# Kernel optimization log

Measured on AMD Instinct MI355X. Metric: run time of the kernel, lower is better.

## Reference

```python
import jax, jax.numpy as jnp
import numpy as np

LAM = 0.5          # lambda_ in DyGCN
GROUPS = 4
EPS_GN = 1e-5
EPS_LN = 1e-5


def _group_norm(y, w, b):
    # y: [B, Ch, N, T]; GroupNorm over (channels-in-group, N, T)
    B, Ch, N, T = y.shape
    yr = y.reshape(B, GROUPS, Ch // GROUPS, N, T)
    mu = yr.mean(axis=(2, 3, 4), keepdims=True)
    var = yr.var(axis=(2, 3, 4), keepdims=True)
    yn = ((yr - mu) * jax.lax.rsqrt(var + EPS_GN)).reshape(B, Ch, N, T)
    return yn * w[None, :, None, None] + b[None, :, None, None]


def _gtu(X, w, b, pw, pb, qw, qb):
    # grouped conv2d, kernel (1,k), stride 1, VALID; out channels = 2*H
    xc = jax.lax.conv_general_dilated(
        X, w, window_strides=(1, 1), padding='VALID',
        feature_group_count=GROUPS,
        dimension_numbers=('NCHW', 'OIHW', 'NCHW'))
    xc = xc + b[None, :, None, None]
    H = X.shape[1]
    xp = _group_norm(xc[:, :H], pw, pb)   # matches torch chunk(2, dim=1)
    xq = _group_norm(xc[:, H:], qw, qb)
    mish = xp * jnp.tanh(jax.nn.softplus(xp))   # Mish
    gate = jnp.clip(xq, 0.0, 1.0)               # Hardtanh(0,1)
    return mish * gate


def reference(x, static_adj, U1, U2, U3, be, Ve, W0, b0, masks, Ws, bs, Wd, bd,
              conv3_w, conv5_w, conv7_w, conv9_w, conv_b,
              gn_pw, gn_pb, gn_qw, gn_qb, fc_w, fc_b, res_w, res_b, ln_w, ln_b):
    B, N, C, T = x.shape
    # ---- Temporal attention ----
    lhs = jnp.einsum('btc,cn->btn', jnp.einsum('bnct,n->btc', x, U1), U2)  # [B,T,N]
    rhs = jnp.einsum('c,bnct->bnt', U3, x)                                 # [B,N,T]
    product = jnp.einsum('btn,bns->bts', lhs, rhs)                          # [B,T,T]
    E = jnp.einsum('ij,bjk->bik', Ve, jax.nn.sigmoid(product + be))
    At = jax.nn.softmax(E, axis=1)
    x_TAt = jnp.einsum('bmt,bts->bms', x.reshape(B, N * C, T), At).reshape(B, N, C, T)
    # ---- DyGCN, vectorized across T ----
    xt = jnp.moveaxis(x_TAt, -1, 1)                                        # [B,T,N,C]
    x0 = jnp.einsum('btnc,hc->btnh', xt, W0) + b0                          # shared linear
    enh = static_adj[None] * jax.nn.sigmoid(masks)                         # [T,N,N]
    s = jnp.einsum('tnm,btmc->btnc', enh, xt)
    static_out = jnp.einsum('btnc,thc->btnh', s, Ws) + bs[None, :, None, :]
    # dynamic branch (DynamicGCNLayer): data-dependent adjacency
    scores = jnp.einsum('btnc,btmc->btnm', xt, xt) / jnp.sqrt(jnp.float32(C))
    adj = jax.nn.softmax(scores, axis=-1)                                  # [B,T,N,N]
    d = jnp.einsum('btnm,btmc->btnc', adj, xt)
    dyn_out = jnp.einsum('btnc,thc->btnh', d, Wd) + bd[None, :, None, :]
    fused = (LAM - 0.025) * static_out + (1.0 - LAM - 0.025) * dyn_out + 0.05 * x0
    X = jnp.transpose(fused, (0, 3, 2, 1))                                 # [B,H,N,T]
    # ---- multi-scale gated temporal convs ----
    outs = [
        _gtu(X, conv3_w, conv_b[0], gn_pw[0], gn_pb[0], gn_qw[0], gn_qb[0]),
        _gtu(X, conv5_w, conv_b[1], gn_pw[1], gn_pb[1], gn_qw[1], gn_qb[1]),
        _gtu(X, conv7_w, conv_b[2], gn_pw[2], gn_pb[2], gn_qw[2], gn_qb[2]),
        _gtu(X, conv9_w, conv_b[3], gn_pw[3], gn_pb[3], gn_qw[3], gn_qb[3]),
    ]
    tc = jnp.concatenate(outs, axis=-1)                                    # [B,H,N,4T-20]
    tc = jnp.einsum('bhnk,ok->bhno', tc, fc_w) + fc_b                      # fcmy (dropout=eval no-op)
    tco = jax.nn.relu(tc)                                                  # [B,H,N,T]
    # ---- residual + LayerNorm ----
    residual = jnp.einsum('bnct,hc->bhnt', x, res_w) + res_b[None, :, None, None]
    y = jax.nn.relu(residual + tco)                                        # [B,H,N,T]
    yp = jnp.transpose(y, (0, 3, 2, 1))                                    # [B,T,N,H]
    mu = yp.mean(axis=-1, keepdims=True)
    var = yp.var(axis=-1, keepdims=True)
    yn = (yp - mu) * jax.lax.rsqrt(var + EPS_LN) * ln_w + ln_b
    return jnp.transpose(yn, (0, 2, 3, 1))                                 # [B,N,H,T]


def setup_inputs():
    key = jax.random.key(0)
    ks = jax.random.split(key, 32)
    B, N, C, T, H = 16, 512, 64, 12, 64
    w = 0.05
    A = jax.random.uniform(ks[0], (N, N), jnp.float32)
    A = A / A.sum(axis=-1, keepdims=True)  # row-normalized static adjacency
    return {
        'x': jax.random.normal(ks[1], (B, N, C, T), jnp.float32),
        'static_adj': A,
        'U1': jax.random.normal(ks[2], (N,), jnp.float32) * w,
        'U2': jax.random.normal(ks[3], (C, N), jnp.float32) * w,
        'U3': jax.random.normal(ks[4], (C,), jnp.float32) * w,
        'be': jax.random.normal(ks[5], (1, T, T), jnp.float32) * w,
        'Ve': jax.random.normal(ks[6], (T, T), jnp.float32) * w,
        'W0': jax.random.normal(ks[7], (H, C), jnp.float32) * w,
        'b0': jnp.zeros((H,), jnp.float32),
        'masks': jax.random.uniform(ks[8], (T, N, N), jnp.float32, 0.8, 1.2),
        'Ws': jax.random.normal(ks[9], (T, H, C), jnp.float32) * w,
        'bs': jnp.zeros((T, H), jnp.float32),
        'Wd': jax.random.normal(ks[10], (T, H, C), jnp.float32) * w,
        'bd': jnp.zeros((T, H), jnp.float32),
        'conv3_w': jax.random.normal(ks[11], (2 * H, H // 4, 1, 3), jnp.float32) * w,
        'conv5_w': jax.random.normal(ks[12], (2 * H, H // 4, 1, 5), jnp.float32) * w,
        'conv7_w': jax.random.normal(ks[13], (2 * H, H // 4, 1, 7), jnp.float32) * w,
        'conv9_w': jax.random.normal(ks[14], (2 * H, H // 4, 1, 9), jnp.float32) * w,
        'conv_b': jnp.zeros((4, 2 * H), jnp.float32),
        'gn_pw': jnp.ones((4, H), jnp.float32),
        'gn_pb': jnp.zeros((4, H), jnp.float32),
        'gn_qw': jnp.ones((4, H), jnp.float32),
        'gn_qb': jnp.zeros((4, H), jnp.float32),
        'fc_w': jax.random.normal(ks[15], (T, 4 * T - 20), jnp.float32) * w,
        'fc_b': jnp.zeros((T,), jnp.float32),
        'res_w': jax.random.normal(ks[16], (H, C), jnp.float32) * w,
        'res_b': jnp.zeros((H,), jnp.float32),
        'ln_w': jnp.ones((H,), jnp.float32),
        'ln_b': jnp.zeros((H,), jnp.float32),
    }
```

## Files before the change

kernel.cpp:

```cpp
#include <hip/hip_runtime.h>

constexpr int Bb = 16, Nn = 512, Cc = 64, Tt = 12, Hh = 64;
constexpr int NCT = Nn * Cc * Tt;
constexpr int CT  = Cc * Tt;

__global__ void k0_rest(const float* __restrict__ rw, float* __restrict__ resT) {
    int i = blockIdx.x * 256 + threadIdx.x;
    if (i < Hh * Cc) {
        int h = i >> 6, c = i & 63;
        resT[c * 64 + h] = rw[i];
    }
}

__global__ void k1a_tmp1(const float* __restrict__ x, const float* __restrict__ U1,
                         float* __restrict__ tmp1) {
    int blk = blockIdx.x;
    int b = blk / 12; int r = blk % 12;
    int ctb = r >> 2; int nch = r & 3;
    int ct = ctb * 256 + threadIdx.x;
    const float* xb = x + (size_t)b * NCT;
    float acc = 0.f;
    int n0 = nch * 128;
    for (int n = n0; n < n0 + 128; ++n)
        acc += xb[n * CT + ct] * U1[n];
    atomicAdd(&tmp1[b * CT + ct], acc);
}

__global__ void k1b_rhs(const float* __restrict__ x, const float* __restrict__ U3,
                        float* __restrict__ rhs) {
    int wid = blockIdx.x * 4 + (threadIdx.x >> 6);
    int b = wid >> 9; int n = wid & 511;
    int l = threadIdx.x & 63;
    const float4* x4 = (const float4*)(x + (size_t)(b * Nn + n) * CT);
    float4 a0 = x4[3 * l], a1 = x4[3 * l + 1], a2 = x4[3 * l + 2];
    float xv[12] = {a0.x,a0.y,a0.z,a0.w, a1.x,a1.y,a1.z,a1.w, a2.x,a2.y,a2.z,a2.w};
    float u = U3[l];
    float p[12];
    #pragma unroll
    for (int t = 0; t < 12; ++t) p[t] = u * xv[t];
    #pragma unroll
    for (int off = 1; off < 64; off <<= 1) {
        #pragma unroll
        for (int t = 0; t < 12; ++t) p[t] += __shfl_xor(p[t], off);
    }
    if (l == 0) {
        float* rp = rhs + (size_t)(b * Nn + n) * 12;
        *(float4*)(rp)     = make_float4(p[0], p[1], p[2], p[3]);
        *(float4*)(rp + 4) = make_float4(p[4], p[5], p[6], p[7]);
        *(float4*)(rp + 8) = make_float4(p[8], p[9], p[10], p[11]);
    }
}

__global__ void k1c_lhs(const float* __restrict__ tmp1, const float* __restrict__ U2,
                        float* __restrict__ lhG) {
    __shared__ float t1[CT];
    int b = blockIdx.x >> 1; int nn = (blockIdx.x & 1) * 256 + threadIdx.x;
    for (int i = threadIdx.x; i < CT; i += 256) t1[i] = tmp1[b * CT + i];
    __syncthreads();
    float l[Tt];
    #pragma unroll
    for (int t = 0; t < Tt; ++t) l[t] = 0.f;
    for (int c = 0; c < Cc; ++c) {
        float u2 = U2[c * Nn + nn];
        #pragma unroll
        for (int t = 0; t < Tt; ++t) l[t] += t1[c * Tt + t] * u2;
    }
    #pragma unroll
    for (int t = 0; t < Tt; ++t) lhG[(size_t)(b * Tt + t) * Nn + nn] = l[t];
}

__global__ void k1c_att(const float* __restrict__ lhG, const float* __restrict__ rhs,
                        const float* __restrict__ be, const float* __restrict__ Ve,
                        float* __restrict__ At) {
    __shared__ float rh[Nn * Tt];
    __shared__ float lh[Tt * Nn];
    __shared__ float part[576];
    __shared__ float sp[144];
    __shared__ float Ee[144];
    int b = blockIdx.x, tid = threadIdx.x;
    for (int i = tid; i < Nn * Tt; i += 256) rh[i] = rhs[b * Nn * Tt + i];
    for (int i = tid; i < Tt * Nn; i += 256) lh[i] = lhG[(size_t)b * Tt * Nn + i];
    __syncthreads();
    for (int task = tid; task < 576; task += 256) {
        int ts = task >> 2, ch = task & 3;
        int t = ts / 12, s2 = ts % 12;
        int n0 = ch * 128;
        float a = 0.f;
        for (int nn = n0; nn < n0 + 128; ++nn) a += lh[t * Nn + nn] * rh[nn * Tt + s2];
        part[task] = a;
    }
    __syncthreads();
    if (tid < 144) {
        float a = part[tid * 4] + part[tid * 4 + 1] + part[tid * 4 + 2] + part[tid * 4 + 3]
                + be[tid];
        sp[tid] = 1.f / (1.f + __expf(-a));
    }
    __syncthreads();
    if (tid < 144) {
        int i = tid / 12, k = tid % 12;
        float a = 0.f;
        #pragma unroll
        for (int j = 0; j < 12; ++j) a += Ve[i * 12 + j] * sp[j * 12 + k];
        Ee[tid] = a;
    }
    __syncthreads();
    if (tid < 12) {
        int k = tid;
        float mx = -1e30f;
        #pragma unroll
        for (int i = 0; i < 12; ++i) mx = fmaxf(mx, Ee[i * 12 + k]);
        float su = 0.f; float ex[12];
        #pragma unroll
        for (int i = 0; i < 12; ++i) { ex[i] = __expf(Ee[i * 12 + k] - mx); su += ex[i]; }
        float inv = 1.f / su;
        #pragma unroll
        for (int i = 0; i < 12; ++i) At[b * 144 + i * 12 + k] = ex[i] * inv;
    }
}

__global__ void k2_xtt(const float* __restrict__ x, const float* __restrict__ At,
                       float* __restrict__ xtN) {
    int idx = blockIdx.x * 256 + threadIdx.x;
    int c = idx & 63; int n = (idx >> 6) & 511; int b = idx >> 15;
    const float4* x4 = (const float4*)(x + (size_t)((b * Nn + n) * Cc + c) * Tt);
    float4 a0 = x4[0], a1 = x4[1], a2 = x4[2];
    float xv[12] = {a0.x,a0.y,a0.z,a0.w, a1.x,a1.y,a1.z,a1.w, a2.x,a2.y,a2.z,a2.w};
    const float* Ab = At + b * 144;
    float* op = xtN + (size_t)b * Tt * Nn * Cc + n * Cc + c;
    #pragma unroll
    for (int t = 0; t < Tt; ++t) {
        float a = 0.f;
        #pragma unroll
        for (int u = 0; u < Tt; ++u) a += xv[u] * Ab[u * 12 + t];
        op[(size_t)t * Nn * Cc] = a;
    }
}

__global__ void k2b_enh(const float* __restrict__ adj, const float* __restrict__ masks,
                        float* __restrict__ enhT) {
    __shared__ float tile[32][33];
    int blk = blockIdx.x;
    int t = blk >> 8; int r = blk & 255;
    int n0 = (r >> 4) * 32; int m0 = (r & 15) * 32;
    int tx = threadIdx.x & 31; int ty = threadIdx.x >> 5;
    #pragma unroll
    for (int i = 0; i < 4; ++i) {
        int nl = ty + 8 * i;
        float a  = adj[(n0 + nl) * Nn + m0 + tx];
        float mk = masks[t * Nn * Nn + (n0 + nl) * Nn + m0 + tx];
        tile[nl][tx] = a / (1.f + __expf(-mk));
    }
    __syncthreads();
    #pragma unroll
    for (int i = 0; i < 4; ++i) {
        int ml = ty + 8 * i;
        enhT[(size_t)(t * Nn + m0 + ml) * Nn + n0 + tx] = tile[tx][ml];
    }
}

__global__ __launch_bounds__(256) __attribute__((amdgpu_waves_per_eu(1, 3)))
void k3_gcn(
    const float* __restrict__ xtN, const float* __restrict__ enhT,
    const float* __restrict__ W0, const float* __restrict__ b0,
    const float* __restrict__ Ws, const float* __restrict__ bs,
    const float* __restrict__ Wd, const float* __restrict__ bd,
    float* __restrict__ F) {
    __shared__ float xs[64][64];
    int blk = (blockIdx.x & 7) * 96 + (blockIdx.x >> 3);
    int seg = blk & 3; int t = (blk >> 2) % Tt; int b = blk / 48;
    int tid = threadIdx.x;
    int lane = tid & 63;
    int w = tid >> 6;
    int half = lane >> 5;
    int r = lane & 31;
    int n = seg * 128 + w * 32 + r;
    int c0 = half * 32;
    const float* xb = xtN + (size_t)(b * Tt + t) * Nn * Cc;
    float row[32];
    {
        const float4* r4 = (const float4*)(xb + n * Cc + c0);
        #pragma unroll
        for (int jj = 0; jj < 8; ++jj) {
            float4 a = r4[jj];
            row[jj*4] = a.x; row[jj*4+1] = a.y; row[jj*4+2] = a.z; row[jj*4+3] = a.w;
        }
    }
    float accd[32], accs[32];
    #pragma unroll
    for (int j = 0; j < 32; ++j) { accd[j] = 0.f; accs[j] = 0.f; }
    float sumexp = 0.f;
    const float* eh = enhT + (size_t)t * Nn * Nn + n;
    for (int m0 = 0; m0 < Nn; m0 += 64) {
        __syncthreads();
        {
            const float4* src = (const float4*)(xb + m0 * Cc);
            float4* dst = (float4*)&xs[0][0];
            #pragma unroll
            for (int i = 0; i < 4; ++i) dst[i * 256 + tid] = src[i * 256 + tid];
        }
        __syncthreads();
        #pragma unroll 1
        for (int m = 0; m < 64; ++m) {
            const float4* vp = (const float4*)&xs[m][c0];
            float4 v0 = vp[0], v1 = vp[1], v2 = vp[2], v3 = vp[3];
            float4 v4 = vp[4], v5 = vp[5], v6 = vp[6], v7 = vp[7];
            float sa, sb;
            sa = row[0]*v0.x + row[1]*v0.y + row[2]*v0.z + row[3]*v0.w
               + row[4]*v1.x + row[5]*v1.y + row[6]*v1.z + row[7]*v1.w
               + row[8]*v2.x + row[9]*v2.y + row[10]*v2.z + row[11]*v2.w
               + row[12]*v3.x + row[13]*v3.y + row[14]*v3.z + row[15]*v3.w;
            sb = row[16]*v4.x + row[17]*v4.y + row[18]*v4.z + row[19]*v4.w
               + row[20]*v5.x + row[21]*v5.y + row[22]*v5.z + row[23]*v5.w
               + row[24]*v6.x + row[25]*v6.y + row[26]*v6.z + row[27]*v6.w
               + row[28]*v7.x + row[29]*v7.y + row[30]*v7.z + row[31]*v7.w;
            float s = sa + sb;
            s += __shfl_xor(s, 32);
            float p = __expf(s * 0.125f);
            sumexp += p;
            float e = eh[(size_t)(m0 + m) * Nn];
            accd[0]  += p*v0.x; accd[1]  += p*v0.y; accd[2]  += p*v0.z; accd[3]  += p*v0.w;
            accd[4]  += p*v1.x; accd[5]  += p*v1.y; accd[6]  += p*v1.z; accd[7]  += p*v1.w;
            accd[8]  += p*v2.x; accd[9]  += p*v2.y; accd[10] += p*v2.z; accd[11] += p*v2.w;
            accd[12] += p*v3.x; accd[13] += p*v3.y; accd[14] += p*v3.z; accd[15] += p*v3.w;
            accd[16] += p*v4.x; accd[17] += p*v4.y; accd[18] += p*v4.z; accd[19] += p*v4.w;
            accd[20] += p*v5.x; accd[21] += p*v5.y; accd[22] += p*v5.z; accd[23] += p*v5.w;
            accd[24] += p*v6.x; accd[25] += p*v6.y; accd[26] += p*v6.z; accd[27] += p*v6.w;
            accd[28] += p*v7.x; accd[29] += p*v7.y; accd[30] += p*v7.z; accd[31] += p*v7.w;
            accs[0]  += e*v0.x; accs[1]  += e*v0.y; accs[2]  += e*v0.z; accs[3]  += e*v0.w;
            accs[4]  += e*v1.x; accs[5]  += e*v1.y; accs[6]  += e*v1.z; accs[7]  += e*v1.w;
            accs[8]  += e*v2.x; accs[9]  += e*v2.y; accs[10] += e*v2.z; accs[11] += e*v2.w;
            accs[12] += e*v3.x; accs[13] += e*v3.y; accs[14] += e*v3.z; accs[15] += e*v3.w;
            accs[16] += e*v4.x; accs[17] += e*v4.y; accs[18] += e*v4.z; accs[19] += e*v4.w;
            accs[20] += e*v5.x; accs[21] += e*v5.y; accs[22] += e*v5.z; accs[23] += e*v5.w;
            accs[24] += e*v6.x; accs[25] += e*v6.y; accs[26] += e*v6.z; accs[27] += e*v6.w;
            accs[28] += e*v7.x; accs[29] += e*v7.y; accs[30] += e*v7.z; accs[31] += e*v7.w;
        }
    }
    float invd = 0.475f / sumexp;
    #pragma unroll
    for (int j = 0; j < 32; ++j) {
        accd[j] *= invd; accs[j] *= 0.475f; row[j] *= 0.05f;
    }
    const float* Wst = Ws + t * Hh * Cc;
    const float* Wdt = Wd + t * Hh * Cc;
    float* Fp = F + ((size_t)(b * Tt + t) * Nn + n) * Hh;
    for (int hb = 0; hb < 16; ++hb) {
        float oo[4];
        #pragma unroll
        for (int k = 0; k < 4; ++k) {
            int h = hb * 4 + k;
            const float4* w04 = (const float4*)(W0 + h * Cc + c0);
            const float4* ws4 = (const float4*)(Wst + h * Cc + c0);
            const float4* wd4 = (const float4*)(Wdt + h * Cc + c0);
            float a = 0.f;
            #pragma unroll
            for (int jj = 0; jj < 8; ++jj) {
                float4 wv = w04[jj], sv = ws4[jj], dv = wd4[jj];
                a += row[jj*4+0]*wv.x + row[jj*4+1]*wv.y + row[jj*4+2]*wv.z + row[jj*4+3]*wv.w;
                a += accs[jj*4+0]*sv.x + accs[jj*4+1]*sv.y + accs[jj*4+2]*sv.z + accs[jj*4+3]*sv.w;
                a += accd[jj*4+0]*dv.x + accd[jj*4+1]*dv.y + accd[jj*4+2]*dv.z + accd[jj*4+3]*dv.w;
            }
            a += __shfl_xor(a, 32);
            oo[k] = a + 0.05f * b0[h] + 0.475f * (bs[t * Hh + h] + bd[t * Hh + h]);
        }
        if ((hb >> 3) == half)
            *(float4*)(Fp + hb * 4) = make_float4(oo[0], oo[1], oo[2], oo[3]);
    }
}

__global__ __launch_bounds__(512) void k4_conv(
                        const float* __restrict__ F,
                        const float* __restrict__ w3, const float* __restrict__ w5,
                        const float* __restrict__ w7, const float* __restrict__ w9,
                        const float* __restrict__ cb,
                        float* __restrict__ xc, float* __restrict__ stats) {
    __shared__ float fl[4 * Tt * Hh];
    __shared__ float sstat[64];
    int blk = blockIdx.x;
    int b = blk >> 7; int n0 = (blk & 127) * 4;
    int tid = threadIdx.x;
    if (tid < 64) sstat[tid] = 0.f;
    for (int i = tid; i < 3072; i += 512) {
        int t = i >> 8; int r = i & 255;
        fl[i] = F[(size_t)(b * Tt + t) * Nn * Hh + n0 * Hh + r];
    }
    __syncthreads();
    int nl = tid >> 7; int co = tid & 127;
    int g = co >> 5;
    float a3[10], a5[8], a7[6], a9[4];
    {
        float c3 = cb[co], c5 = cb[128 + co], c7 = cb[256 + co], c9 = cb[384 + co];
        #pragma unroll
        for (int j = 0; j < 10; ++j) a3[j] = c3;
        #pragma unroll
        for (int j = 0; j < 8; ++j) a5[j] = c5;
        #pragma unroll
        for (int j = 0; j < 6; ++j) a7[j] = c7;
        #pragma unroll
        for (int j = 0; j < 4; ++j) a9[j] = c9;
    }
    for (int ci = 0; ci < 16; ++ci) {
        int cig = g * 16 + ci;
        float xr[12];
        #pragma unroll
        for (int tt = 0; tt < 12; ++tt) xr[tt] = fl[tt * 256 + nl * 64 + cig];
        const float* p3 = w3 + (co * 16 + ci) * 3;
        #pragma unroll
        for (int dt = 0; dt < 3; ++dt) {
            float wv = p3[dt];
            #pragma unroll
            for (int j = 0; j < 10; ++j) a3[j] += xr[j + dt] * wv;
        }
        const float* p5 = w5 + (co * 16 + ci) * 5;
        #pragma unroll
        for (int dt = 0; dt < 5; ++dt) {
            float wv = p5[dt];
            #pragma unroll
            for (int j = 0; j < 8; ++j) a5[j] += xr[j + dt] * wv;
        }
        const float* p7 = w7 + (co * 16 + ci) * 7;
        #pragma unroll
        for (int dt = 0; dt < 7; ++dt) {
            float wv = p7[dt];
            #pragma unroll
            for (int j = 0; j < 6; ++j) a7[j] += xr[j + dt] * wv;
        }
        const float* p9 = w9 + (co * 16 + ci) * 9;
        #pragma unroll
        for (int dt = 0; dt < 9; ++dt) {
            float wv = p9[dt];
            #pragma unroll
            for (int j = 0; j < 4; ++j) a9[j] += xr[j + dt] * wv;
        }
    }
    int pg = (co < 64) ? (co >> 4) : 4 + ((co - 64) >> 4);
    float* xcw = xc + (size_t)(b * Nn + n0 + nl) * 28 * 128 + co;
    float su, sq;
    su = 0.f; sq = 0.f;
    #pragma unroll
    for (int j = 0; j < 10; ++j) { float v = a3[j]; xcw[j * 128] = v; su += v; sq += v * v; }
    #pragma unroll
    for (int off = 1; off < 16; off <<= 1) { su += __shfl_xor(su, off); sq += __shfl_xor(sq, off); }
    if ((tid & 15) == 0) { atomicAdd(&sstat[(0 * 8 + pg) * 2], su); atomicAdd(&sstat[(0 * 8 + pg) * 2 + 1], sq); }
    su = 0.f; sq = 0.f;
    #pragma unroll
    for (int j = 0; j < 8; ++j) { float v = a5[j]; xcw[(10 + j) * 128] = v; su += v; sq += v * v; }
    #pragma unroll
    for (int off = 1; off < 16; off <<= 1) { su += __shfl_xor(su, off); sq += __shfl_xor(sq, off); }
    if ((tid & 15) == 0) { atomicAdd(&sstat[(1 * 8 + pg) * 2], su); atomicAdd(&sstat[(1 * 8 + pg) * 2 + 1], sq); }
    su = 0.f; sq = 0.f;
    #pragma unroll
    for (int j = 0; j < 6; ++j) { float v = a7[j]; xcw[(18 + j) * 128] = v; su += v; sq += v * v; }
    #pragma unroll
    for (int off = 1; off < 16; off <<= 1) { su += __shfl_xor(su, off); sq += __shfl_xor(sq, off); }
    if ((tid & 15) == 0) { atomicAdd(&sstat[(2 * 8 + pg) * 2], su); atomicAdd(&sstat[(2 * 8 + pg) * 2 + 1], sq); }
    su = 0.f; sq = 0.f;
    #pragma unroll
    for (int j = 0; j < 4; ++j) { float v = a9[j]; xcw[(24 + j) * 128] = v; su += v; sq += v * v; }
    #pragma unroll
    for (int off = 1; off < 16; off <<= 1) { su += __shfl_xor(su, off); sq += __shfl_xor(sq, off); }
    if ((tid & 15) == 0) { atomicAdd(&sstat[(3 * 8 + pg) * 2], su); atomicAdd(&sstat[(3 * 8 + pg) * 2 + 1], sq); }
    __syncthreads();
    if (tid < 64) {
        int s = tid >> 4; int pgq = (tid >> 1) & 7; int st = tid & 1;
        atomicAdd(&stats[((s * Bb + b) * 8 + pgq) * 2 + st], sstat[(s * 8 + pgq) * 2 + st]);
    }
}

__global__ __launch_bounds__(256) void k5_final(
                         const float* __restrict__ xc, const float* __restrict__ stats,
                         const float* __restrict__ x,
                         const float* __restrict__ gpw, const float* __restrict__ gpb,
                         const float* __restrict__ gqw, const float* __restrict__ gqb,
                         const float* __restrict__ fcw, const float* __restrict__ fcb,
                         const float* __restrict__ resT, const float* __restrict__ rb,
                         const float* __restrict__ lnw, const float* __restrict__ lnb,
                         float* __restrict__ out) {
    int blk = blockIdx.x;
    int b = blk >> 7; int n = (blk & 127) * 4 + (threadIdx.x >> 6);
    int h = threadIdx.x & 63;
    int pg = h >> 4;
    const int TkA[4] = {10, 8, 6, 4};
    float mu_p[4], rs_p[4], mu_q[4], rs_q[4];
    #pragma unroll
    for (int s = 0; s < 4; ++s) {
        float cnt = 16.f * 512.f * (float)TkA[s];
        float su = stats[((s * Bb + b) * 8 + pg) * 2];
        float sq = stats[((s * Bb + b) * 8 + pg) * 2 + 1];
        float mu = su / cnt; float var = sq / cnt - mu * mu;
        mu_p[s] = mu; rs_p[s] = rsqrtf(var + 1e-5f);
        su = stats[((s * Bb + b) * 8 + 4 + pg) * 2];
        sq = stats[((s * Bb + b) * 8 + 4 + pg) * 2 + 1];
        mu = su / cnt; var = sq / cnt - mu * mu;
        mu_q[s] = mu; rs_q[s] = rsqrtf(var + 1e-5f);
    }
    const float* xcp = xc + (size_t)(b * Nn + n) * 28 * 128;
    float pb_[28], qb_[28];
    #pragma unroll
    for (int k = 0; k < 28; ++k) {
        pb_[k] = xcp[k * 128 + h];
        qb_[k] = xcp[k * 128 + 64 + h];
    }
    float tc[28];
    int off = 0;
    #pragma unroll
    for (int s = 0; s < 4; ++s) {
        float pw = gpw[s * 64 + h], pbv = gpb[s * 64 + h];
        float qw = gqw[s * 64 + h], qbv = gqb[s * 64 + h];
        #pragma unroll
        for (int j = 0; j < 10; ++j) {
            if (j < TkA[s]) {
                float p = (pb_[off + j] - mu_p[s]) * rs_p[s] * pw + pbv;
                float q = (qb_[off + j] - mu_q[s]) * rs_q[s] * qw + qbv;
                float mish;
                if (p > 20.f) mish = p;
                else { float z = 1.f + __expf(p); float z2 = z * z; mish = p * (z2 - 1.f) / (z2 + 1.f); }
                float gate = fminf(fmaxf(q, 0.f), 1.f);
                tc[off + j] = mish * gate;
            }
        }
        off += TkA[s];
    }
    float o[12];
    #pragma unroll
    for (int t = 0; t < 12; ++t) {
        float a = fcb[t];
        #pragma unroll
        for (int k = 0; k < 28; ++k) a += tc[k] * fcw[t * 28 + k];
        o[t] = fmaxf(a, 0.f);
    }
    const float* xr = x + (size_t)(b * Nn + n) * CT;
    float res[12];
    float rbv = rb[h];
    #pragma unroll
    for (int t = 0; t < 12; ++t) res[t] = rbv;
    for (int c = 0; c < 64; ++c) {
        float rv = resT[c * 64 + h];
        #pragma unroll
        for (int t = 0; t < 12; ++t) res[t] += xr[c * 12 + t] * rv;
    }
    float y[12];
    #pragma unroll
    for (int t = 0; t < 12; ++t) y[t] = fmaxf(res[t] + o[t], 0.f);
    float lw = lnw[h], lb = lnb[h];
    float ov[12];
    #pragma unroll
    for (int t = 0; t < 12; ++t) {
        float s1 = y[t], s2 = y[t] * y[t];
        #pragma unroll
        for (int o2 = 32; o2 > 0; o2 >>= 1) {
            s1 += __shfl_xor(s1, o2);
            s2 += __shfl_xor(s2, o2);
        }
        float mu = s1 * (1.f / 64.f);
        float var = s2 * (1.f / 64.f) - mu * mu;
        ov[t] = (y[t] - mu) * rsqrtf(var + 1e-5f) * lw + lb;
    }
    float* op = out + ((size_t)(b * Nn + n) * Hh + h) * Tt;
    *(float4*)(op)     = make_float4(ov[0], ov[1], ov[2], ov[3]);
    *(float4*)(op + 4) = make_float4(ov[4], ov[5], ov[6], ov[7]);
    *(float4*)(op + 8) = make_float4(ov[8], ov[9], ov[10], ov[11]);
}

extern "C" void kernel_launch(void* const* d_in, const int* in_sizes, int n_in,
                              void* d_out, int out_size, void* d_ws, size_t ws_size,
                              hipStream_t stream) {
    const float* x    = (const float*)d_in[0];
    const float* adj  = (const float*)d_in[1];
    const float* U1   = (const float*)d_in[2];
    const float* U2   = (const float*)d_in[3];
    const float* U3   = (const float*)d_in[4];
    const float* be   = (const float*)d_in[5];
    const float* Ve   = (const float*)d_in[6];
    const float* W0   = (const float*)d_in[7];
    const float* b0   = (const float*)d_in[8];
    const float* masks= (const float*)d_in[9];
    const float* Ws   = (const float*)d_in[10];
    const float* bs   = (const float*)d_in[11];
    const float* Wd   = (const float*)d_in[12];
    const float* bd   = (const float*)d_in[13];
    const float* w3   = (const float*)d_in[14];
    const float* w5   = (const float*)d_in[15];
    const float* w7   = (const float*)d_in[16];
    const float* w9   = (const float*)d_in[17];
    const float* cb   = (const float*)d_in[18];
    const float* gpw  = (const float*)d_in[19];
    const float* gpb  = (const float*)d_in[20];
    const float* gqw  = (const float*)d_in[21];
    const float* gqb  = (const float*)d_in[22];
    const float* fcw  = (const float*)d_in[23];
    const float* fcb  = (const float*)d_in[24];
    const float* rw   = (const float*)d_in[25];
    const float* rb   = (const float*)d_in[26];
    const float* lnw  = (const float*)d_in[27];
    const float* lnb  = (const float*)d_in[28];
    float* out = (float*)d_out;
    float* ws  = (float*)d_ws;

    float* tmp1  = ws;
    float* stats = ws + 12288;
    float* At    = ws + 13312;
    float* rhs   = ws + 15616;
    float* resT  = ws + 113920;
    float* xtN   = ws + 118016;
    float* enhT  = ws + 6409472;
    float* F     = ws + 9555200;
    float* xc    = ws + 15846656;
    float* lhG   = xtN;

    hipMemsetAsync(ws, 0, 13312 * sizeof(float), stream);

    k0_rest<<<16, 256, 0, stream>>>(rw, resT);
    k1a_tmp1<<<192, 256, 0, stream>>>(x, U1, tmp1);
    k1b_rhs<<<2048, 256, 0, stream>>>(x, U3, rhs);
    k2b_enh<<<3072, 256, 0, stream>>>(adj, masks, enhT);
    k1c_lhs<<<32, 256, 0, stream>>>(tmp1, U2, lhG);
    k1c_att<<<16, 256, 0, stream>>>(lhG, rhs, be, Ve, At);
    k2_xtt<<<2048, 256, 0, stream>>>(x, At, xtN);
    k3_gcn<<<768, 256, 0, stream>>>(xtN, enhT, W0, b0, Ws, bs, Wd, bd, F);
    k4_conv<<<2048, 512, 0, stream>>>(F, w3, w5, w7, w9, cb, xc, stats);
    k5_final<<<2048, 256, 0, stream>>>(xc, stats, x, gpw, gpb, gqw, gqb,
                                       fcw, fcb, resT, rb, lnw, lnb, out);
}
```

Before: 1.405 ms.

## Split GCN channels four ways per node and stage enhanced adjacency in LDS

The GCN kernel now gives each node to four lanes with 16 channels each instead of two lanes with 32, halving per-thread accumulator registers. The grid doubles to 1536 blocks of 64 nodes, and the occupancy hint is raised to 4 waves per EU. The enhanced-adjacency tile is now loaded cooperatively into shared memory with float4 loads instead of strided per-thread global reads. In exchange there is an extra shuffle per reduction, twice the xs tile reloads across blocks, and more LDS per block.

```diff
diff --git a/kernel.cpp b/kernel.cpp
--- a/kernel.cpp
+++ b/kernel.cpp
@@ -158,7 +158,7 @@
     }
 }
 
-__global__ __launch_bounds__(256) __attribute__((amdgpu_waves_per_eu(1, 3)))
+__global__ __launch_bounds__(256) __attribute__((amdgpu_waves_per_eu(4)))
 void k3_gcn(
     const float* __restrict__ xtN, const float* __restrict__ enhT,
     const float* __restrict__ W0, const float* __restrict__ b0,
@@ -166,30 +166,32 @@
     const float* __restrict__ Wd, const float* __restrict__ bd,
     float* __restrict__ F) {
     __shared__ float xs[64][64];
-    int blk = (blockIdx.x & 7) * 96 + (blockIdx.x >> 3);
-    int seg = blk & 3; int t = (blk >> 2) % Tt; int b = blk / 48;
+    __shared__ float es[64][64];
+    int blk = (blockIdx.x & 7) * 192 + (blockIdx.x >> 3);
+    int seg = blk & 7; int t = (blk >> 3) % Tt; int b = blk / 96;
     int tid = threadIdx.x;
     int lane = tid & 63;
     int w = tid >> 6;
-    int half = lane >> 5;
-    int r = lane & 31;
-    int n = seg * 128 + w * 32 + r;
-    int c0 = half * 32;
+    int cg = lane >> 4;
+    int r = lane & 15;
+    int nl = w * 16 + r;
+    int n = seg * 64 + nl;
+    int c0 = cg * 16;
     const float* xb = xtN + (size_t)(b * Tt + t) * Nn * Cc;
-    float row[32];
+    const float* eb = enhT + (size_t)t * Nn * Nn + seg * 64;
+    float row[16];
     {
         const float4* r4 = (const float4*)(xb + n * Cc + c0);
         #pragma unroll
-        for (int jj = 0; jj < 8; ++jj) {
+        for (int jj = 0; jj < 4; ++jj) {
             float4 a = r4[jj];
             row[jj*4] = a.x; row[jj*4+1] = a.y; row[jj*4+2] = a.z; row[jj*4+3] = a.w;
         }
     }
-    float accd[32], accs[32];
-    #pragma unroll
-    for (int j = 0; j < 32; ++j) { accd[j] = 0.f; accs[j] = 0.f; }
+    float accd[16], accs[16];
+    #pragma unroll
+    for (int j = 0; j < 16; ++j) { accd[j] = 0.f; accs[j] = 0.f; }
     float sumexp = 0.f;
-    const float* eh = enhT + (size_t)t * Nn * Nn + n;
     for (int m0 = 0; m0 < Nn; m0 += 64) {
         __syncthreads();
         {
@@ -198,47 +200,44 @@
             #pragma unroll
             for (int i = 0; i < 4; ++i) dst[i * 256 + tid] = src[i * 256 + tid];
         }
+        {
+            #pragma unroll
+            for (int i = 0; i < 4; ++i) {
+                int f = i * 256 + tid;
+                int m = f >> 4; int q = f & 15;
+                *(float4*)&es[m][q * 4] =
+                    *(const float4*)(eb + (size_t)(m0 + m) * Nn + q * 4);
+            }
+        }
         __syncthreads();
         #pragma unroll 1
         for (int m = 0; m < 64; ++m) {
             const float4* vp = (const float4*)&xs[m][c0];
             float4 v0 = vp[0], v1 = vp[1], v2 = vp[2], v3 = vp[3];
-            float4 v4 = vp[4], v5 = vp[5], v6 = vp[6], v7 = vp[7];
             float sa, sb;
             sa = row[0]*v0.x + row[1]*v0.y + row[2]*v0.z + row[3]*v0.w
-               + row[4]*v1.x + row[5]*v1.y + row[6]*v1.z + row[7]*v1.w
-               + row[8]*v2.x + row[9]*v2.y + row[10]*v2.z + row[11]*v2.w
+               + row[4]*v1.x + row[5]*v1.y + row[6]*v1.z + row[7]*v1.w;
+            sb = row[8]*v2.x + row[9]*v2.y + row[10]*v2.z + row[11]*v2.w
                + row[12]*v3.x + row[13]*v3.y + row[14]*v3.z + row[15]*v3.w;
-            sb = row[16]*v4.x + row[17]*v4.y + row[18]*v4.z + row[19]*v4.w
-               + row[20]*v5.x + row[21]*v5.y + row[22]*v5.z + row[23]*v5.w
-               + row[24]*v6.x + row[25]*v6.y + row[26]*v6.z + row[27]*v6.w
-               + row[28]*v7.x + row[29]*v7.y + row[30]*v7.z + row[31]*v7.w;
             float s = sa + sb;
+            s += __shfl_xor(s, 16);
             s += __shfl_xor(s, 32);
             float p = __expf(s * 0.125f);
             sumexp += p;
-            float e = eh[(size_t)(m0 + m) * Nn];
+            float e = es[m][nl];
             accd[0]  += p*v0.x; accd[1]  += p*v0.y; accd[2]  += p*v0.z; accd[3]  += p*v0.w;
             accd[4]  += p*v1.x; accd[5]  += p*v1.y; accd[6]  += p*v1.z; accd[7]  += p*v1.w;
             accd[8]  += p*v2.x; accd[9]  += p*v2.y; accd[10] += p*v2.z; accd[11] += p*v2.w;
             accd[12] += p*v3.x; accd[13] += p*v3.y; accd[14] += p*v3.z; accd[15] += p*v3.w;
-            accd[16] += p*v4.x; accd[17] += p*v4.y; accd[18] += p*v4.z; accd[19] += p*v4.w;
-            accd[20] += p*v5.x; accd[21] += p*v5.y; accd[22] += p*v5.z; accd[23] += p*v5.w;
-            accd[24] += p*v6.x; accd[25] += p*v6.y; accd[26] += p*v6.z; accd[27] += p*v6.w;
-            accd[28] += p*v7.x; accd[29] += p*v7.y; accd[30] += p*v7.z; accd[31] += p*v7.w;
             accs[0]  += e*v0.x; accs[1]  += e*v0.y; accs[2]  += e*v0.z; accs[3]  += e*v0.w;
             accs[4]  += e*v1.x; accs[5]  += e*v1.y; accs[6]  += e*v1.z; accs[7]  += e*v1.w;
             accs[8]  += e*v2.x; accs[9]  += e*v2.y; accs[10] += e*v2.z; accs[11] += e*v2.w;
             accs[12] += e*v3.x; accs[13] += e*v3.y; accs[14] += e*v3.z; accs[15] += e*v3.w;
-            accs[16] += e*v4.x; accs[17] += e*v4.y; accs[18] += e*v4.z; accs[19] += e*v4.w;
-            accs[20] += e*v5.x; accs[21] += e*v5.y; accs[22] += e*v5.z; accs[23] += e*v5.w;
-            accs[24] += e*v6.x; accs[25] += e*v6.y; accs[26] += e*v6.z; accs[27] += e*v6.w;
-            accs[28] += e*v7.x; accs[29] += e*v7.y; accs[30] += e*v7.z; accs[31] += e*v7.w;
         }
     }
     float invd = 0.475f / sumexp;
     #pragma unroll
-    for (int j = 0; j < 32; ++j) {
+    for (int j = 0; j < 16; ++j) {
         accd[j] *= invd; accs[j] *= 0.475f; row[j] *= 0.05f;
     }
     const float* Wst = Ws + t * Hh * Cc;
@@ -254,16 +253,17 @@
             const float4* wd4 = (const float4*)(Wdt + h * Cc + c0);
             float a = 0.f;
             #pragma unroll
-            for (int jj = 0; jj < 8; ++jj) {
+            for (int jj = 0; jj < 4; ++jj) {
                 float4 wv = w04[jj], sv = ws4[jj], dv = wd4[jj];
                 a += row[jj*4+0]*wv.x + row[jj*4+1]*wv.y + row[jj*4+2]*wv.z + row[jj*4+3]*wv.w;
                 a += accs[jj*4+0]*sv.x + accs[jj*4+1]*sv.y + accs[jj*4+2]*sv.z + accs[jj*4+3]*sv.w;
                 a += accd[jj*4+0]*dv.x + accd[jj*4+1]*dv.y + accd[jj*4+2]*dv.z + accd[jj*4+3]*dv.w;
             }
+            a += __shfl_xor(a, 16);
             a += __shfl_xor(a, 32);
             oo[k] = a + 0.05f * b0[h] + 0.475f * (bs[t * Hh + h] + bd[t * Hh + h]);
         }
-        if ((hb >> 3) == half)
+        if ((hb >> 2) == cg)
             *(float4*)(Fp + hb * 4) = make_float4(oo[0], oo[1], oo[2], oo[3]);
     }
 }
@@ -517,7 +517,7 @@
     k1c_lhs<<<32, 256, 0, stream>>>(tmp1, U2, lhG);
     k1c_att<<<16, 256, 0, stream>>>(lhG, rhs, be, Ve, At);
     k2_xtt<<<2048, 256, 0, stream>>>(x, At, xtN);
-    k3_gcn<<<768, 256, 0, stream>>>(xtN, enhT, W0, b0, Ws, bs, Wd, bd, F);
+    k3_gcn<<<1536, 256, 0, stream>>>(xtN, enhT, W0, b0, Ws, bs, Wd, bd, F);
     k4_conv<<<2048, 512, 0, stream>>>(F, w3, w5, w7, w9, cb, xc, stats);
     k5_final<<<2048, 256, 0, stream>>>(xc, stats, x, gpw, gpb, gqw, gqb,
                                        fcw, fcb, resT, rb, lnw, lnb, out);
```

After: 1.549 ms. 10.3% more time.
